# Performance work log

Hardware: AMD Instinct MI355X
Metric: run time of the kernel (lower is better)

The kernel has to match this reference:

```python
import jax, jax.numpy as jnp
import numpy as np

B, S, D, H, W = 4, 2048, 512, 8, 16
DK = D // H


def setup_inputs() -> dict:
    key = jax.random.key(0)
    ks = jax.random.split(key, 11)
    scale = 1.0 / np.sqrt(D)
    return {
        "query": jax.random.normal(ks[0], (B, S, D), jnp.float32),
        "key": jax.random.normal(ks[1], (B, S, D), jnp.float32),
        "value": jax.random.normal(ks[2], (B, S, D), jnp.float32),
        "Wq": jax.random.normal(ks[3], (D, D), jnp.float32) * scale,
        "bq": jnp.zeros((D,), jnp.float32),
        "Wk": jax.random.normal(ks[4], (D, D), jnp.float32) * scale,
        "bk": jnp.zeros((D,), jnp.float32),
        "Wv": jax.random.normal(ks[5], (D, D), jnp.float32) * scale,
        "bv": jnp.zeros((D,), jnp.float32),
        "Wo": jax.random.normal(ks[6], (D, D), jnp.float32) * scale,
        "bo": jnp.zeros((D,), jnp.float32),
    }


def reference(query, key, value, Wq, bq, Wk, bk, Wv, bv, Wo, bo):
    b, s, d = query.shape
    # QKV projections -> [b, H, s, DK]
    Q = (query @ Wq + bq).reshape(b, s, H, DK).transpose(0, 2, 1, 3)
    K = (key @ Wk + bk).reshape(b, s, H, DK).transpose(0, 2, 1, 3)
    V = (value @ Wv + bv).reshape(b, s, H, DK).transpose(0, 2, 1, 3)
    # Dense scores (faithful to original O(n^2) math), then static band mask
    scores = jnp.einsum("bhqd,bhkd->bhqk", Q, K) / jnp.sqrt(jnp.array(DK, scores_dtype := Q.dtype))
    idx = jnp.arange(s)
    local = jnp.abs(idx[:, None] - idx[None, :]) <= W  # [s, s] band
    mask_value = jnp.finfo(scores.dtype).min
    scores = jnp.where(local[None, None], scores, mask_value)
    attn = jax.nn.softmax(scores, axis=-1)
    ctx = jnp.einsum("bhqk,bhkd->bhqd", attn, V)
    ctx = ctx.transpose(0, 2, 1, 3).reshape(b, s, d)
    return ctx @ Wo + bo
```

## Files before the change

### kernel.cpp

```cpp
#include <hip/hip_runtime.h>

typedef __attribute__((ext_vector_type(8))) short bf16x8;
typedef __attribute__((ext_vector_type(4))) float f32x4;
typedef __attribute__((ext_vector_type(4))) unsigned int u32x4;
typedef __attribute__((ext_vector_type(8))) unsigned short ushort8;

#define BB 4
#define SS 2048
#define DD 512
#define HH 8
#define DKK 64
#define WWIN 16
#define MTOT (BB*SS)
#define MKE  ((long)MTOT*DD)
#define NKE  ((long)DD*DD)

__device__ __forceinline__ unsigned short f2bf(float f) {
  unsigned int u = __float_as_uint(f);
  u += 0x7fffu + ((u >> 16) & 1u);
  return (unsigned short)(u >> 16);
}
__device__ __forceinline__ float bf2f(unsigned short s) {
  return __uint_as_float(((unsigned int)s) << 16);
}

__device__ __forceinline__ void gload_lds16(const unsigned short* g, unsigned short* l) {
  __builtin_amdgcn_global_load_lds((const __attribute__((address_space(1))) void*)g,
                                   (__attribute__((address_space(3))) void*)l, 16, 0, 0);
}

__global__ __launch_bounds__(256) void convert_x(
    const float* __restrict__ q, const float* __restrict__ k, const float* __restrict__ v,
    const float* __restrict__ bq, const float* __restrict__ bk, const float* __restrict__ bv,
    unsigned short* __restrict__ xbf, float* __restrict__ bias_all)
{
  long idx = (long)blockIdx.x * 256 + threadIdx.x;
  if (idx < 3*DD) {
    bias_all[idx] = idx < DD ? bq[idx] : (idx < 2*DD ? bk[idx-DD] : bv[idx-2*DD]);
  }
  long e = idx * 8;
  const long SZ = MKE;
  const float* s; long t = e;
  if (t < SZ) { s = q; }
  else if (t < 2*SZ) { s = k; t -= SZ; }
  else { s = v; t -= 2*SZ; }
  float4 a  = *(const float4*)(s + t);
  float4 b2 = *(const float4*)(s + t + 4);
  ushort8 o;
  o[0]=f2bf(a.x);  o[1]=f2bf(a.y);  o[2]=f2bf(a.z);  o[3]=f2bf(a.w);
  o[4]=f2bf(b2.x); o[5]=f2bf(b2.y); o[6]=f2bf(b2.z); o[7]=f2bf(b2.w);
  *(ushort8*)(xbf + e) = o;
}

__global__ __launch_bounds__(256) void convert_w(
    const float* __restrict__ Wq, const float* __restrict__ Wk,
    const float* __restrict__ Wv, const float* __restrict__ Wo,
    unsigned short* __restrict__ wt)
{
  int bx = blockIdx.x;
  int wm = bx >> 6;
  int tile = bx & 63;
  int tr = tile >> 3, tc = tile & 7;
  const float* src = wm==0 ? Wq : wm==1 ? Wk : wm==2 ? Wv : Wo;
  unsigned short* dst = wt + (long)wm*NKE;
  __shared__ float tl[64][65];
  int t = threadIdx.x;
  int cr = t >> 6;
  int cc = t & 63;
  for (int p = 0; p < 16; ++p) {
    int row = p*4 + cr;
    tl[row][cc] = src[(long)(tr*64+row)*DD + tc*64 + cc];
  }
  __syncthreads();
  for (int p = 0; p < 16; ++p) {
    int orow = p*4 + cr;
    dst[(long)(tc*64 + orow)*DD + tr*64 + cc] = f2bf(tl[cc][orow]);
  }
}

template<int OUT_BF16>
__global__ __launch_bounds__(256, 2) void gemm_kernel(
    const unsigned short* __restrict__ Abase, long aZ,
    const unsigned short* __restrict__ Btbase, long bZ,
    const float* __restrict__ biasBase, long biasZ,
    void* __restrict__ outBase, long outZ,
    int M, int N, int K)
{
  const int z = blockIdx.z;
  const unsigned short* A  = Abase  + (long)z*aZ;
  const unsigned short* Bt = Btbase + (long)z*bZ;
  const float* bias = biasBase + (long)z*biasZ;

  const int tid  = threadIdx.x;
  const int lane = tid & 63;
  const int w    = tid >> 6;
  const int wr   = w >> 1, wc = w & 1;
  const int m0   = blockIdx.y * 128;
  const int n0   = blockIdx.x * 128;

  __shared__ unsigned short lA[128*64];
  __shared__ unsigned short lB[128*64];

  f32x4 acc[4][4] = {};

  for (int kt = 0; kt < K; kt += 64) {
    for (int i = 0; i < 4; ++i) {
      int e   = (w*4+i)*512 + lane*8;
      int row = e >> 6, col = e & 63;
      gload_lds16(A  + (long)(m0 + row)*K + kt + col, &lA[(w*4+i)*512]);
      gload_lds16(Bt + (long)(n0 + row)*K + kt + col, &lB[(w*4+i)*512]);
    }
    __syncthreads();
    for (int kk = 0; kk < 2; ++kk) {
      bf16x8 af[4], bfr[4];
      for (int m = 0; m < 4; ++m) {
        int row = wr*64 + m*16 + (lane & 15);
        af[m] = *reinterpret_cast<const bf16x8*>(&lA[row*64 + kk*32 + (lane>>4)*8]);
      }
      for (int n = 0; n < 4; ++n) {
        int col = wc*64 + n*16 + (lane & 15);
        bfr[n] = *reinterpret_cast<const bf16x8*>(&lB[col*64 + kk*32 + (lane>>4)*8]);
      }
      for (int m = 0; m < 4; ++m)
        for (int n = 0; n < 4; ++n)
          acc[m][n] = __builtin_amdgcn_mfma_f32_16x16x32_bf16(af[m], bfr[n], acc[m][n], 0, 0, 0);
    }
    __syncthreads();
  }

  for (int m = 0; m < 4; ++m) {
    int rbase = m0 + wr*64 + m*16 + ((lane>>4)<<2);
    for (int n = 0; n < 4; ++n) {
      int col = n0 + wc*64 + n*16 + (lane & 15);
      float bv = bias[col];
      for (int r = 0; r < 4; ++r) {
        float val = acc[m][n][r] + bv;
        long idx = (long)z*outZ + (long)(rbase + r)*N + col;
        if (OUT_BF16) ((unsigned short*)outBase)[idx] = f2bf(val);
        else          ((float*)outBase)[idx] = val;
      }
    }
  }
}

#define KP 76
#define PP 76
__global__ __launch_bounds__(256) void attn_kernel(
    const unsigned short* __restrict__ Qbf, const unsigned short* __restrict__ Kbf,
    const unsigned short* __restrict__ Vbf, unsigned short* __restrict__ ctxbf)
{
  const int q0 = blockIdx.x * 128;
  const int h  = blockIdx.y;
  const int b  = blockIdx.z;
  const int tid = threadIdx.x, lane = tid & 63, w = tid >> 6;
  const int c = lane & 15, g = lane >> 4;
  const int w0 = q0 - WWIN;

  __shared__ unsigned short K_l[160*KP];
  __shared__ unsigned short V_l[160*KP];
  __shared__ unsigned short P_l[4][32*PP];

  const long baseRow = (long)b*SS*DD + (long)h*DKK;

  for (int i = 0; i < 5; ++i) {
    int u = i*256 + tid;
    int row = u >> 3, c8 = (u & 7) * 8;
    int gk = w0 + row;
    u32x4 kv = {0,0,0,0}, vv = {0,0,0,0};
    if (gk >= 0 && gk < SS) {
      kv = *(const u32x4*)(Kbf + baseRow + (long)gk*DD + c8);
      vv = *(const u32x4*)(Vbf + baseRow + (long)gk*DD + c8);
    }
    *(u32x4*)(&K_l[row*KP + c8]) = kv;
    *(u32x4*)(&V_l[row*KP + c8]) = vv;
  }
  __syncthreads();

  const int qw0   = q0 + w*32;
  const int kbase = w*32;

  bf16x8 aq[2][2];
  for (int m = 0; m < 2; ++m)
    for (int kk = 0; kk < 2; ++kk)
      aq[m][kk] = *reinterpret_cast<const bf16x8*>(
          Qbf + baseRow + (long)(qw0 + m*16 + c)*DD + kk*32 + g*8);

  f32x4 accs[2][4] = {};
  for (int kk = 0; kk < 2; ++kk) {
    bf16x8 bk[4];
    for (int n = 0; n < 4; ++n)
      bk[n] = *reinterpret_cast<const bf16x8*>(&K_l[(kbase + n*16 + c)*KP + kk*32 + g*8]);
    for (int m = 0; m < 2; ++m)
      for (int n = 0; n < 4; ++n)
        accs[m][n] = __builtin_amdgcn_mfma_f32_16x16x32_bf16(aq[m][kk], bk[n], accs[m][n], 0, 0, 0);
  }

  float pden[2][4];
  for (int m = 0; m < 2; ++m) {
    for (int r = 0; r < 4; ++r) {
      int qi = m*16 + g*4 + r;
      float sv[4];
      float mx = -INFINITY;
      for (int n = 0; n < 4; ++n) {
        int kr = n*16 + c;
        int d  = kr - qi;
        int kg = w0 + kbase + kr;
        bool ok = (d >= 0) && (d <= 2*WWIN) && (kg >= 0) && (kg < SS);
        sv[n] = ok ? accs[m][n][r] * 0.125f : -INFINITY;
        mx = fmaxf(mx, sv[n]);
      }
      for (int off = 1; off < 16; off <<= 1) mx = fmaxf(mx, __shfl_xor(mx, off, 64));
      float sum = 0.f;
      for (int n = 0; n < 4; ++n) {
        float e = __expf(sv[n] - mx);
        sum += e;
        P_l[w][(m*16 + g*4 + r)*PP + n*16 + c] = f2bf(e);
      }
      for (int off = 1; off < 16; off <<= 1) sum += __shfl_xor(sum, off, 64);
      pden[m][r] = sum;
    }
  }
  __syncthreads();

  f32x4 acco[2][4] = {};
  for (int kk = 0; kk < 2; ++kk) {
    bf16x8 pa[2];
    for (int m = 0; m < 2; ++m)
      pa[m] = *reinterpret_cast<const bf16x8*>(&P_l[w][(m*16 + c)*PP + kk*32 + g*8]);
    bf16x8 bv[4];
    int kb = kbase + kk*32 + g*8;
    for (int n = 0; n < 4; ++n) {
      ushort8 t;
      for (int j = 0; j < 8; ++j) t[j] = V_l[(kb + j)*KP + n*16 + c];
      bv[n] = *reinterpret_cast<bf16x8*>(&t);
    }
    for (int m = 0; m < 2; ++m)
      for (int n = 0; n < 4; ++n)
        acco[m][n] = __builtin_amdgcn_mfma_f32_16x16x32_bf16(pa[m], bv[n], acco[m][n], 0, 0, 0);
  }

  for (int m = 0; m < 2; ++m) {
    for (int r = 0; r < 4; ++r) {
      int q = qw0 + m*16 + g*4 + r;
      float inv = 1.f / pden[m][r];
      for (int n = 0; n < 4; ++n)
        ctxbf[baseRow + (long)q*DD + n*16 + c] = f2bf(acco[m][n][r] * inv);
    }
  }
}

extern "C" void kernel_launch(void* const* d_in, const int* in_sizes, int n_in,
                              void* d_out, int out_size, void* d_ws, size_t ws_size,
                              hipStream_t stream) {
  const float* q  = (const float*)d_in[0];
  const float* k  = (const float*)d_in[1];
  const float* v  = (const float*)d_in[2];
  const float* Wq = (const float*)d_in[3];
  const float* bq = (const float*)d_in[4];
  const float* Wk = (const float*)d_in[5];
  const float* bk = (const float*)d_in[6];
  const float* Wv = (const float*)d_in[7];
  const float* bv = (const float*)d_in[8];
  const float* Wo = (const float*)d_in[9];
  const float* bo = (const float*)d_in[10];

  char* ws = (char*)d_ws;
  unsigned short* xbf   = (unsigned short*)(ws);
  unsigned short* wtbf  = (unsigned short*)(ws + 25165824);
  float*          bias_all = (float*)(ws + 27262976);
  unsigned short* qkvbf = (unsigned short*)(ws + 27269120);
  unsigned short* ctxbf = (unsigned short*)(ws + 52434944);

  convert_x<<<6144, 256, 0, stream>>>(q, k, v, bq, bk, bv, xbf, bias_all);
  convert_w<<<256, 256, 0, stream>>>(Wq, Wk, Wv, Wo, wtbf);
  gemm_kernel<1><<<dim3(4, 64, 3), 256, 0, stream>>>(
      xbf, MKE, wtbf, NKE, bias_all, DD,
      (void*)qkvbf, MKE, MTOT, DD, DD);
  attn_kernel<<<dim3(SS/128, HH, BB), 256, 0, stream>>>(
      qkvbf, qkvbf + MKE, qkvbf + 2*MKE, ctxbf);
  gemm_kernel<0><<<dim3(4, 64, 1), 256, 0, stream>>>(
      ctxbf, 0, wtbf + 3*NKE, 0, bo, 0,
      (void*)d_out, 0, MTOT, DD, DD);
}
```

Baseline: 158.8 us.

## Fuse fp32-to-bf16 activation conversion into QKV GEMM A-tile load

Removes the separate convert_x kernel and has the QKV GEMM read fp32 activations directly, converting to bf16 while staging A tiles into LDS. The bias copy moves into extra blocks of convert_w. This avoids writing and re-reading the 24MB bf16 copy of the inputs and drops one launch, but the A load now goes through registers instead of direct global-to-LDS loads, and each A tile is re-converted by all four N-blocks. The attention kernel also hoists the Q loads above the K/V staging and raises wave priority around its MFMA sections.

Result: no change. 160.8 us (+1.3%).

```diff
diff --git a/kernel.cpp b/kernel.cpp
--- a/kernel.cpp
+++ b/kernel.cpp
@@ -3,7 +3,8 @@
 typedef __attribute__((ext_vector_type(8))) short bf16x8;
 typedef __attribute__((ext_vector_type(4))) float f32x4;
 typedef __attribute__((ext_vector_type(4))) unsigned int u32x4;
-typedef __attribute__((ext_vector_type(8))) unsigned short ushort8;
+typedef __attribute__((ext_vector_type(8))) unsigned short bfu8;
+typedef __attribute__((ext_vector_type(4))) unsigned short bfu4;
 
 #define BB 4
 #define SS 2048
@@ -29,35 +30,18 @@
                                    (__attribute__((address_space(3))) void*)l, 16, 0, 0);
 }
 
-__global__ __launch_bounds__(256) void convert_x(
-    const float* __restrict__ q, const float* __restrict__ k, const float* __restrict__ v,
-    const float* __restrict__ bq, const float* __restrict__ bk, const float* __restrict__ bv,
-    unsigned short* __restrict__ xbf, float* __restrict__ bias_all)
-{
-  long idx = (long)blockIdx.x * 256 + threadIdx.x;
-  if (idx < 3*DD) {
-    bias_all[idx] = idx < DD ? bq[idx] : (idx < 2*DD ? bk[idx-DD] : bv[idx-2*DD]);
-  }
-  long e = idx * 8;
-  const long SZ = MKE;
-  const float* s; long t = e;
-  if (t < SZ) { s = q; }
-  else if (t < 2*SZ) { s = k; t -= SZ; }
-  else { s = v; t -= 2*SZ; }
-  float4 a  = *(const float4*)(s + t);
-  float4 b2 = *(const float4*)(s + t + 4);
-  ushort8 o;
-  o[0]=f2bf(a.x);  o[1]=f2bf(a.y);  o[2]=f2bf(a.z);  o[3]=f2bf(a.w);
-  o[4]=f2bf(b2.x); o[5]=f2bf(b2.y); o[6]=f2bf(b2.z); o[7]=f2bf(b2.w);
-  *(ushort8*)(xbf + e) = o;
-}
-
 __global__ __launch_bounds__(256) void convert_w(
     const float* __restrict__ Wq, const float* __restrict__ Wk,
     const float* __restrict__ Wv, const float* __restrict__ Wo,
-    unsigned short* __restrict__ wt)
+    const float* __restrict__ bq, const float* __restrict__ bk, const float* __restrict__ bv,
+    unsigned short* __restrict__ wt, float* __restrict__ bias_all)
 {
   int bx = blockIdx.x;
+  if (bx >= 256) {
+    int idx = (bx - 256) * 256 + threadIdx.x;
+    bias_all[idx] = idx < DD ? bq[idx] : (idx < 2*DD ? bk[idx-DD] : bv[idx-2*DD]);
+    return;
+  }
   int wm = bx >> 6;
   int tile = bx & 63;
   int tr = tile >> 3, tc = tile & 7;
@@ -78,16 +62,16 @@
   }
 }
 
-template<int OUT_BF16>
+template<int OUT_BF16, int A_FP32>
 __global__ __launch_bounds__(256, 2) void gemm_kernel(
-    const unsigned short* __restrict__ Abase, long aZ,
+    const void* __restrict__ a0, const void* __restrict__ a1, const void* __restrict__ a2,
     const unsigned short* __restrict__ Btbase, long bZ,
     const float* __restrict__ biasBase, long biasZ,
     void* __restrict__ outBase, long outZ,
     int M, int N, int K)
 {
   const int z = blockIdx.z;
-  const unsigned short* A  = Abase  + (long)z*aZ;
+  const void* Av = z==0 ? a0 : z==1 ? a1 : a2;
   const unsigned short* Bt = Btbase + (long)z*bZ;
   const float* bias = biasBase + (long)z*biasZ;
 
@@ -107,8 +91,25 @@
     for (int i = 0; i < 4; ++i) {
       int e   = (w*4+i)*512 + lane*8;
       int row = e >> 6, col = e & 63;
-      gload_lds16(A  + (long)(m0 + row)*K + kt + col, &lA[(w*4+i)*512]);
       gload_lds16(Bt + (long)(n0 + row)*K + kt + col, &lB[(w*4+i)*512]);
+    }
+    if (A_FP32) {
+      const float* Afp = (const float*)Av;
+      for (int i = 0; i < 8; ++i) {
+        int e   = (i*256 + tid) * 4;
+        int row = e >> 6, col = e & 63;
+        float4 f = *(const float4*)(Afp + (long)(m0 + row)*K + kt + col);
+        bfu4 o;
+        o[0]=f2bf(f.x); o[1]=f2bf(f.y); o[2]=f2bf(f.z); o[3]=f2bf(f.w);
+        *(bfu4*)(&lA[e]) = o;
+      }
+    } else {
+      const unsigned short* A = (const unsigned short*)Av;
+      for (int i = 0; i < 4; ++i) {
+        int e   = (w*4+i)*512 + lane*8;
+        int row = e >> 6, col = e & 63;
+        gload_lds16(A + (long)(m0 + row)*K + kt + col, &lA[(w*4+i)*512]);
+      }
     }
     __syncthreads();
     for (int kk = 0; kk < 2; ++kk) {
@@ -161,6 +162,14 @@
   __shared__ unsigned short P_l[4][32*PP];
 
   const long baseRow = (long)b*SS*DD + (long)h*DKK;
+  const int qw0   = q0 + w*32;
+  const int kbase = w*32;
+
+  bf16x8 aq[2][2];
+  for (int m = 0; m < 2; ++m)
+    for (int kk = 0; kk < 2; ++kk)
+      aq[m][kk] = *reinterpret_cast<const bf16x8*>(
+          Qbf + baseRow + (long)(qw0 + m*16 + c)*DD + kk*32 + g*8);
 
   for (int i = 0; i < 5; ++i) {
     int u = i*256 + tid;
@@ -176,16 +185,8 @@
   }
   __syncthreads();
 
-  const int qw0   = q0 + w*32;
-  const int kbase = w*32;
-
-  bf16x8 aq[2][2];
-  for (int m = 0; m < 2; ++m)
-    for (int kk = 0; kk < 2; ++kk)
-      aq[m][kk] = *reinterpret_cast<const bf16x8*>(
-          Qbf + baseRow + (long)(qw0 + m*16 + c)*DD + kk*32 + g*8);
-
   f32x4 accs[2][4] = {};
+  __builtin_amdgcn_s_setprio(1);
   for (int kk = 0; kk < 2; ++kk) {
     bf16x8 bk[4];
     for (int n = 0; n < 4; ++n)
@@ -194,6 +195,7 @@
       for (int n = 0; n < 4; ++n)
         accs[m][n] = __builtin_amdgcn_mfma_f32_16x16x32_bf16(aq[m][kk], bk[n], accs[m][n], 0, 0, 0);
   }
+  __builtin_amdgcn_s_setprio(0);
 
   float pden[2][4];
   for (int m = 0; m < 2; ++m) {
@@ -230,13 +232,15 @@
     bf16x8 bv[4];
     int kb = kbase + kk*32 + g*8;
     for (int n = 0; n < 4; ++n) {
-      ushort8 t;
+      bfu8 t;
       for (int j = 0; j < 8; ++j) t[j] = V_l[(kb + j)*KP + n*16 + c];
       bv[n] = *reinterpret_cast<bf16x8*>(&t);
     }
+    __builtin_amdgcn_s_setprio(1);
     for (int m = 0; m < 2; ++m)
       for (int n = 0; n < 4; ++n)
         acco[m][n] = __builtin_amdgcn_mfma_f32_16x16x32_bf16(pa[m], bv[n], acco[m][n], 0, 0, 0);
+    __builtin_amdgcn_s_setprio(0);
   }
 
   for (int m = 0; m < 2; ++m) {
@@ -265,20 +269,18 @@
   const float* bo = (const float*)d_in[10];
 
   char* ws = (char*)d_ws;
-  unsigned short* xbf   = (unsigned short*)(ws);
-  unsigned short* wtbf  = (unsigned short*)(ws + 25165824);
-  float*          bias_all = (float*)(ws + 27262976);
-  unsigned short* qkvbf = (unsigned short*)(ws + 27269120);
-  unsigned short* ctxbf = (unsigned short*)(ws + 52434944);
-
-  convert_x<<<6144, 256, 0, stream>>>(q, k, v, bq, bk, bv, xbf, bias_all);
-  convert_w<<<256, 256, 0, stream>>>(Wq, Wk, Wv, Wo, wtbf);
-  gemm_kernel<1><<<dim3(4, 64, 3), 256, 0, stream>>>(
-      xbf, MKE, wtbf, NKE, bias_all, DD,
+  unsigned short* wtbf     = (unsigned short*)(ws);
+  float*          bias_all = (float*)(ws + 2097152);
+  unsigned short* qkvbf    = (unsigned short*)(ws + 2103296);
+  unsigned short* ctxbf    = (unsigned short*)(ws + 27269120);
+
+  convert_w<<<262, 256, 0, stream>>>(Wq, Wk, Wv, Wo, bq, bk, bv, wtbf, bias_all);
+  gemm_kernel<1,1><<<dim3(4, 64, 3), 256, 0, stream>>>(
+      q, k, v, wtbf, NKE, bias_all, DD,
       (void*)qkvbf, MKE, MTOT, DD, DD);
   attn_kernel<<<dim3(SS/128, HH, BB), 256, 0, stream>>>(
       qkvbf, qkvbf + MKE, qkvbf + 2*MKE, ctxbf);
-  gemm_kernel<0><<<dim3(4, 64, 1), 256, 0, stream>>>(
-      ctxbf, 0, wtbf + 3*NKE, 0, bo, 0,
+  gemm_kernel<0,0><<<dim3(4, 64, 1), 256, 0, stream>>>(
+      ctxbf, ctxbf, ctxbf, wtbf + 3*NKE, 0, bo, 0,
       (void*)d_out, 0, MTOT, DD, DD);
 }
```
